# Optimization experiments

Hardware: AMD Instinct MI355X
Metric: run time of the kernel (lower is better)

The kernel has to match this reference:

```python
import jax, jax.numpy as jnp
import numpy as np

SCALE = 64.0 ** -0.5  # dim ** -0.5
H, D = 8, 8  # heads, head_dim (dim = 64)


def setup_inputs() -> dict:
    key = jax.random.key(0)
    ks = jax.random.split(key, 5)
    b, n, dim = 4, 2048, 64
    return {
        "x": jax.random.normal(ks[0], (b, n, dim), dtype=jnp.float32),
        "Wqkv": jax.random.normal(ks[1], (dim, 3 * dim), dtype=jnp.float32) * 0.05,
        "bqkv": jax.random.normal(ks[2], (3 * dim,), dtype=jnp.float32) * 0.05,
        "W1": jax.random.normal(ks[3], (dim, dim), dtype=jnp.float32) * 0.05,
        "b1": jax.random.normal(ks[4], (dim,), dtype=jnp.float32) * 0.05,
    }


def reference(x, Wqkv, bqkv, W1, b1):
    b, n, dim = x.shape
    # --- stage 1: standard multi-head attention ---
    qkv = x @ Wqkv + bqkv  # [b, n, 3*dim]
    q, k, v = jnp.split(qkv, 3, axis=-1)
    # rearrange 'b n (h d) -> b h n d'
    split = lambda t: t.reshape(b, n, H, D).transpose(0, 2, 1, 3)
    q, k, v = split(q), split(k), split(v)
    dots = jnp.einsum('bhid,bhjd->bhij', q, k) * SCALE  # [b,h,n,n]
    attn = jax.nn.softmax(dots, axis=-1)
    out1 = jnp.einsum('bhij,bhjd->bhid', attn, v)
    out = out1.transpose(0, 2, 1, 3).reshape(b, n, dim)  # 'b h n d -> b n (h d)'
    # --- stage 2: second attention on nn1 projection (same weights => q1=k1=v1) ---
    p = out @ W1 + b1  # [b, n, 64]
    # torch: q1.view(b, 8, n, 8) -- a raw reshape, NOT a head split
    q1 = p.reshape(b, 8, n, 8)
    dots1 = jnp.einsum('bhid,bhjd->bhij', q1, q1) * SCALE  # [b,8,n,n]
    attn1 = jax.nn.softmax(dots1, axis=-1)
    out2 = jnp.einsum('bhij,bhjd->bhid', attn1, q1)
    # torch: rearrange 'b h n d -> b n (h d)'
    out2 = out2.transpose(0, 2, 1, 3).reshape(b, n, dim)
    out2 = out2 @ W1 + b1
    # dropout is identity in eval mode
    return out2
```

## Files before the change

kernel.cpp:

```cpp
#include <hip/hip_runtime.h>

typedef __attribute__((ext_vector_type(8))) short s8v;
typedef __attribute__((ext_vector_type(4))) short s4v;
typedef __attribute__((ext_vector_type(4))) float fx4;
typedef unsigned short u16;
typedef unsigned int u32;
typedef unsigned char u8;

#define QK_SCALE 0.1803368801111204f

#if __has_builtin(__builtin_amdgcn_exp2f)
#define EXP2(x) __builtin_amdgcn_exp2f(x)
#else
#define EXP2(x) exp2f(x)
#endif

static __device__ __forceinline__ u16 f2bf(float f) {
    u32 u = __float_as_uint(f);
    u += 0x7fffu + ((u >> 16) & 1u);
    return (u16)(u >> 16);
}
static __device__ __forceinline__ float bf2f(u16 h) {
    return __uint_as_float(((u32)h) << 16);
}
static __device__ __forceinline__ int packtrunc(float a, float b) {
    return (int)__builtin_amdgcn_perm(__float_as_uint(b), __float_as_uint(a), 0x07060302u);
}

static __device__ __forceinline__ fx4 mfma16(s4v a, s4v b, fx4 c) {
#if __has_builtin(__builtin_amdgcn_mfma_f32_16x16x16bf16_1k)
    return __builtin_amdgcn_mfma_f32_16x16x16bf16_1k(a, b, c, 0, 0, 0);
#else
    asm("v_mfma_f32_16x16x16_bf16 %0, %1, %2, %3" : "=v"(c) : "v"(a), "v"(b), "v"(c));
    return c;
#endif
}

__global__ __launch_bounds__(192) void qkv_proj_kernel(
    const float* __restrict__ X, const float* __restrict__ W,
    const float* __restrict__ bias,
    u16* __restrict__ Qh, u16* __restrict__ Kh, u16* __restrict__ Vt,
    u32* __restrict__ VtBoth)
{
    {
        const int gt = blockIdx.x * 192 + threadIdx.x;
        #pragma unroll
        for (int i = 0; i < 3; ++i) {
            const int idx = gt + i * 196608;
            if (idx < 524288) {
                const int region = idx >> 6, word = idx & 63;
                VtBoth[region * 128 + 64 + word] = (word < 8) ? 0x3f803f80u : 0u;
            }
        }
    }
    __shared__ __align__(16) float xsT[64 * 12];
    const int row0 = blockIdx.x * 8;
    const int t = threadIdx.x;
    if (t < 64) {
        #pragma unroll
        for (int r = 0; r < 8; ++r)
            xsT[t * 12 + r] = X[(size_t)(row0 + r) * 64 + t];
    }
    __syncthreads();
    const int j = t;
    const float bj = bias[j];
    float acc[8];
    #pragma unroll
    for (int r = 0; r < 8; ++r) acc[r] = bj;
    #pragma unroll 4
    for (int k = 0; k < 64; ++k) {
        const float w = W[k * 192 + j];
        const float4 x0 = *(const float4*)&xsT[k * 12];
        const float4 x1 = *(const float4*)&xsT[k * 12 + 4];
        acc[0] = fmaf(x0.x, w, acc[0]);
        acc[1] = fmaf(x0.y, w, acc[1]);
        acc[2] = fmaf(x0.z, w, acc[2]);
        acc[3] = fmaf(x0.w, w, acc[3]);
        acc[4] = fmaf(x1.x, w, acc[4]);
        acc[5] = fmaf(x1.y, w, acc[5]);
        acc[6] = fmaf(x1.z, w, acc[6]);
        acc[7] = fmaf(x1.w, w, acc[7]);
    }
    const int c = j & 63;
    const int h = c >> 3, d = c & 7;
    #pragma unroll
    for (int r = 0; r < 8; ++r) {
        const int R = row0 + r;
        const int bi = R >> 11, i = R & 2047;
        const int bh = bi * 8 + h;
        const float v = acc[r];
        if (j < 64) {
            const float qs = v * QK_SCALE;
            const u16 hh = f2bf(qs);
            const u16 ll = f2bf(qs - bf2f(hh));
            u16* qp = Qh + ((size_t)(bh * 2048 + i)) * 16 + d;
            qp[0] = hh; qp[8] = ll;
        } else if (j < 128) {
            const u16 hh = f2bf(v);
            const u16 ll = f2bf(v - bf2f(hh));
            u16* kp = Kh + ((size_t)(bh * 128 + (i >> 4)) * 16 + (i & 15)) * 16 + d;
            kp[0] = hh; kp[8] = ll;
        } else {
            Vt[((size_t)(bh * 128 + (i >> 4)) * 16 + d) * 16 + (i & 15)] = f2bf(v);
        }
    }
}

__global__ __launch_bounds__(256, 4) void attn_mfma5_kernel(
    const u16* __restrict__ Qh, const u8* __restrict__ Khb,
    const u8* __restrict__ Vtb, float* __restrict__ Part)
{
    __shared__ __align__(16) float Lr[4][4][64][4];
    const int bh = blockIdx.x, qt = blockIdx.y, sp = blockIdx.z;
    const int tid = threadIdx.x, w = tid >> 6, l = tid & 63;
    const int g = l >> 4, ql = l & 15;

    s8v bq[4];
    #pragma unroll
    for (int qg = 0; qg < 4; ++qg)
        bq[qg] = *(const s8v*)(Qh + ((size_t)(bh * 2048 + qt * 64 + qg * 16 + ql)) * 16
                               + (g >> 1) * 8);

    const size_t kvoff = (size_t)bh * 65536 + sp * 32768 + w * 8192;
    const u8* kptr = Khb + kvoff + ql * 32 + (g & 1) * 16;
    const u8* vptr = Vtb + kvoff + ql * 32 + g * 8;

    fx4 acc0 = {0.f, 0.f, 0.f, 0.f}, acc1 = acc0, acc2 = acc0, acc3 = acc0;
    const fx4 zf = {0.f, 0.f, 0.f, 0.f};

    s8v k0 = *(const s8v*)(kptr);
    s8v k1 = *(const s8v*)(kptr + 512);
    s4v v0 = *(const s4v*)(vptr);
    s4v v1 = *(const s4v*)(vptr + 512);

#define QK_COMPUTE(KA, VA)                                                      \
    {                                                                           \
        _Pragma("unroll")                                                       \
        for (int qg = 0; qg < 4; ++qg) {                                        \
            fx4 s = __builtin_amdgcn_mfma_f32_16x16x32_bf16(KA, bq[qg], zf, 0, 0, 0); \
            const float e0 = EXP2(s[0]), e1 = EXP2(s[1]);                       \
            const float e2 = EXP2(s[2]), e3 = EXP2(s[3]);                       \
            union { int i[2]; s4v v; } bp;                                      \
            bp.i[0] = packtrunc(e0, e1);                                        \
            bp.i[1] = packtrunc(e2, e3);                                        \
            fx4& acc = (qg == 0) ? acc0 : (qg == 1) ? acc1 : (qg == 2) ? acc2 : acc3; \
            acc = mfma16(VA, bp.v, acc);                                        \
        }                                                                       \
    }

    #pragma unroll 1
    for (int seg = 0; seg < 16; seg += 2) {
        const s8v k2 = *(const s8v*)(kptr + (seg + 2) * 512);
        const s4v v2 = *(const s4v*)(vptr + (seg + 2) * 512);
        const s8v k3 = *(const s8v*)(kptr + (seg + 3) * 512);
        const s4v v3 = *(const s4v*)(vptr + (seg + 3) * 512);
        QK_COMPUTE(k0, v0);
        QK_COMPUTE(k1, v1);
        k0 = k2; v0 = v2; k1 = k3; v1 = v3;
    }
#undef QK_COMPUTE

    *(fx4*)&Lr[w][0][l][0] = acc0;
    *(fx4*)&Lr[w][1][l][0] = acc1;
    *(fx4*)&Lr[w][2][l][0] = acc2;
    *(fx4*)&Lr[w][3][l][0] = acc3;
    __syncthreads();
    fx4 fin = {0.f, 0.f, 0.f, 0.f};
    #pragma unroll
    for (int wp = 0; wp < 4; ++wp) {
        const fx4 v = *(const fx4*)&Lr[wp][w][l][0];
        fin[0] += v[0]; fin[1] += v[1]; fin[2] += v[2]; fin[3] += v[3];
    }

    const int qglob = qt * 64 + w * 16 + ql;
    float* pp = Part + ((size_t)(bh * 2048 + qglob)) * 24 + sp * 12;
    if (g < 2) {
        const float4 o = {fin[0], fin[1], fin[2], fin[3]};
        *(float4*)(pp + g * 4) = o;
    } else if (g == 2) {
        pp[8] = fin[0];
    }
}

__global__ __launch_bounds__(256) void attn_combine2_kernel(
    const float* __restrict__ Part, float* __restrict__ M)
{
    const int idx = blockIdx.x * 256 + threadIdx.x;
    const float* pp = Part + (size_t)idx * 24;
    const float inv = 1.0f / (pp[8] + pp[20]);
    float o[8];
    #pragma unroll
    for (int d = 0; d < 8; ++d) o[d] = (pp[d] + pp[12 + d]) * inv;
    const int bh = idx >> 11, q = idx & 2047;
    const int b = bh >> 3, h = bh & 7;
    float* op = M + ((size_t)(b * 2048 + q)) * 64 + h * 8;
    const float4 o0 = {o[0], o[1], o[2], o[3]};
    const float4 o1 = {o[4], o[5], o[6], o[7]};
    *(float4*)op = o0;
    *(float4*)(op + 4) = o1;
}

__global__ __launch_bounds__(64) void proj64_kernel(
    const float* __restrict__ X, const float* __restrict__ W,
    const float* __restrict__ bias,
    u16* __restrict__ Qh, u16* __restrict__ Kh, u16* __restrict__ Vt,
    float* __restrict__ Out, int mode)
{
    __shared__ __align__(16) float xsT[64 * 12];
    const int row0 = blockIdx.x * 8;
    const int c = threadIdx.x;
    #pragma unroll
    for (int r = 0; r < 8; ++r)
        xsT[c * 12 + r] = X[(size_t)(row0 + r) * 64 + c];
    __syncthreads();
    const float bc = bias[c];
    float acc[8];
    #pragma unroll
    for (int r = 0; r < 8; ++r) acc[r] = bc;
    #pragma unroll 4
    for (int k = 0; k < 64; ++k) {
        const float w = W[k * 64 + c];
        const float4 x0 = *(const float4*)&xsT[k * 12];
        const float4 x1 = *(const float4*)&xsT[k * 12 + 4];
        acc[0] = fmaf(x0.x, w, acc[0]);
        acc[1] = fmaf(x0.y, w, acc[1]);
        acc[2] = fmaf(x0.z, w, acc[2]);
        acc[3] = fmaf(x0.w, w, acc[3]);
        acc[4] = fmaf(x1.x, w, acc[4]);
        acc[5] = fmaf(x1.y, w, acc[5]);
        acc[6] = fmaf(x1.z, w, acc[6]);
        acc[7] = fmaf(x1.w, w, acc[7]);
    }
    if (mode == 0) {
        #pragma unroll
        for (int r = 0; r < 8; ++r) {
            const int R = row0 + r;
            const int bi = R >> 11, rr = R & 2047;
            const int bh = bi * 8 + (rr >> 8);
            const int key = (rr & 255) * 8 + (c >> 3);
            const int d = c & 7;
            const int kg = key >> 4, kr = key & 15;
            const float p = acc[r];
            const float qs = p * QK_SCALE;
            const u16 qh = f2bf(qs);
            const u16 qlo = f2bf(qs - bf2f(qh));
            const u16 kh = f2bf(p);
            const u16 kl = f2bf(p - bf2f(kh));
            u16* qp = Qh + ((size_t)(bh * 2048 + key)) * 16 + d;
            qp[0] = qh; qp[8] = qlo;
            u16* kp = Kh + ((size_t)(bh * 128 + kg) * 16 + kr) * 16 + d;
            kp[0] = kh; kp[8] = kl;
            Vt[((size_t)(bh * 128 + kg) * 16 + d) * 16 + kr] = f2bf(p);
        }
    } else {
        #pragma unroll
        for (int r = 0; r < 8; ++r)
            Out[(size_t)(row0 + r) * 64 + c] = acc[r];
    }
}

extern "C" void kernel_launch(void* const* d_in, const int* in_sizes, int n_in,
                              void* d_out, int out_size, void* d_ws, size_t ws_size,
                              hipStream_t stream) {
    const float* x    = (const float*)d_in[0];
    const float* Wqkv = (const float*)d_in[1];
    const float* bqkv = (const float*)d_in[2];
    const float* W1   = (const float*)d_in[3];
    const float* b1   = (const float*)d_in[4];
    float* out = (float*)d_out;
    u8* w8 = (u8*)d_ws;

    u16*   Qh0  = (u16*)(w8);
    u16*   Kh0  = (u16*)(w8 + (2u << 20));
    u16*   Vt0  = (u16*)(w8 + (4u << 20));
    u16*   Vt1  = (u16*)(w8 + (6u << 20));
    u16*   Qh1  = (u16*)(w8 + (8u << 20));
    u16*   Kh1  = (u16*)(w8 + (10u << 20));
    float* Part = (float*)(w8 + (12u << 20));
    float* M1   = (float*)(w8 + (18u << 20));
    float* M2   = (float*)(w8);

    qkv_proj_kernel<<<1024, 192, 0, stream>>>(x, Wqkv, bqkv, Qh0, Kh0, Vt0, (u32*)Vt0);
    attn_mfma5_kernel<<<dim3(32, 32, 2), 256, 0, stream>>>(Qh0, (const u8*)Kh0, (const u8*)Vt0, Part);
    attn_combine2_kernel<<<256, 256, 0, stream>>>(Part, M1);
    proj64_kernel<<<1024, 64, 0, stream>>>(M1, W1, b1, Qh1, Kh1, Vt1, nullptr, 0);
    attn_mfma5_kernel<<<dim3(32, 32, 2), 256, 0, stream>>>(Qh1, (const u8*)Kh1, (const u8*)Vt1, Part);
    attn_combine2_kernel<<<256, 256, 0, stream>>>(Part, M2);
    proj64_kernel<<<1024, 64, 0, stream>>>(M2, W1, b1, nullptr, nullptr, nullptr, out, 1);
}
```

Measured before the change: 72.95 us.

## Drop KV split-K and fuse softmax normalization into attention kernel

```diff
diff --git a/kernel.cpp b/kernel.cpp
--- a/kernel.cpp
+++ b/kernel.cpp
@@ -30,6 +30,8 @@
 static __device__ __forceinline__ fx4 mfma16(s4v a, s4v b, fx4 c) {
 #if __has_builtin(__builtin_amdgcn_mfma_f32_16x16x16bf16_1k)
     return __builtin_amdgcn_mfma_f32_16x16x16bf16_1k(a, b, c, 0, 0, 0);
+#elif __has_builtin(__builtin_amdgcn_mfma_f32_16x16x16_bf16)
+    return __builtin_amdgcn_mfma_f32_16x16x16_bf16(a, b, c, 0, 0, 0);
 #else
     asm("v_mfma_f32_16x16x16_bf16 %0, %1, %2, %3" : "=v"(c) : "v"(a), "v"(b), "v"(c));
     return c;
@@ -106,26 +108,28 @@
     }
 }
 
-__global__ __launch_bounds__(256, 4) void attn_mfma5_kernel(
+__global__ __launch_bounds__(256, 8) void attn_mfma9_kernel(
     const u16* __restrict__ Qh, const u8* __restrict__ Khb,
-    const u8* __restrict__ Vtb, float* __restrict__ Part)
+    const u8* __restrict__ Vtb, float* __restrict__ M)
 {
-    __shared__ __align__(16) float Lr[4][4][64][4];
-    const int bh = blockIdx.x, qt = blockIdx.y, sp = blockIdx.z;
+    __shared__ __align__(16) float Lr[4][2][64][4];
+    const int bh = blockIdx.x, qt = blockIdx.y;
     const int tid = threadIdx.x, w = tid >> 6, l = tid & 63;
     const int g = l >> 4, ql = l & 15;
 
-    s8v bq[4];
-    #pragma unroll
-    for (int qg = 0; qg < 4; ++qg)
-        bq[qg] = *(const s8v*)(Qh + ((size_t)(bh * 2048 + qt * 64 + qg * 16 + ql)) * 16
+    s8v bq[2];
+    #pragma unroll
+    for (int qg = 0; qg < 2; ++qg)
+        bq[qg] = *(const s8v*)(Qh + ((size_t)(bh * 2048 + qt * 32 + qg * 16 + ql)) * 16
                                + (g >> 1) * 8);
 
-    const size_t kvoff = (size_t)bh * 65536 + sp * 32768 + w * 8192;
+    const size_t kvoff = (size_t)bh * 65536 + w * 16384;
     const u8* kptr = Khb + kvoff + ql * 32 + (g & 1) * 16;
     const u8* vptr = Vtb + kvoff + ql * 32 + g * 8;
 
-    fx4 acc0 = {0.f, 0.f, 0.f, 0.f}, acc1 = acc0, acc2 = acc0, acc3 = acc0;
+    fx4 acc[2];
+    acc[0] = fx4{0.f, 0.f, 0.f, 0.f};
+    acc[1] = fx4{0.f, 0.f, 0.f, 0.f};
     const fx4 zf = {0.f, 0.f, 0.f, 0.f};
 
     s8v k0 = *(const s8v*)(kptr);
@@ -133,71 +137,50 @@
     s4v v0 = *(const s4v*)(vptr);
     s4v v1 = *(const s4v*)(vptr + 512);
 
-#define QK_COMPUTE(KA, VA)                                                      \
+#define PROCESS(KA, VA)                                                         \
     {                                                                           \
         _Pragma("unroll")                                                       \
-        for (int qg = 0; qg < 4; ++qg) {                                        \
+        for (int qg = 0; qg < 2; ++qg) {                                        \
             fx4 s = __builtin_amdgcn_mfma_f32_16x16x32_bf16(KA, bq[qg], zf, 0, 0, 0); \
-            const float e0 = EXP2(s[0]), e1 = EXP2(s[1]);                       \
-            const float e2 = EXP2(s[2]), e3 = EXP2(s[3]);                       \
-            union { int i[2]; s4v v; } bp;                                      \
-            bp.i[0] = packtrunc(e0, e1);                                        \
-            bp.i[1] = packtrunc(e2, e3);                                        \
-            fx4& acc = (qg == 0) ? acc0 : (qg == 1) ? acc1 : (qg == 2) ? acc2 : acc3; \
-            acc = mfma16(VA, bp.v, acc);                                        \
+            union { int i2[2]; s4v v; } bp;                                     \
+            bp.i2[0] = packtrunc(EXP2(s[0]), EXP2(s[1]));                       \
+            bp.i2[1] = packtrunc(EXP2(s[2]), EXP2(s[3]));                       \
+            acc[qg] = mfma16(VA, bp.v, acc[qg]);                                \
         }                                                                       \
     }
 
     #pragma unroll 1
-    for (int seg = 0; seg < 16; seg += 2) {
+    for (int seg = 0; seg < 32; seg += 2) {
         const s8v k2 = *(const s8v*)(kptr + (seg + 2) * 512);
         const s4v v2 = *(const s4v*)(vptr + (seg + 2) * 512);
         const s8v k3 = *(const s8v*)(kptr + (seg + 3) * 512);
         const s4v v3 = *(const s4v*)(vptr + (seg + 3) * 512);
-        QK_COMPUTE(k0, v0);
-        QK_COMPUTE(k1, v1);
+        PROCESS(k0, v0);
+        PROCESS(k1, v1);
         k0 = k2; v0 = v2; k1 = k3; v1 = v3;
     }
-#undef QK_COMPUTE
-
-    *(fx4*)&Lr[w][0][l][0] = acc0;
-    *(fx4*)&Lr[w][1][l][0] = acc1;
-    *(fx4*)&Lr[w][2][l][0] = acc2;
-    *(fx4*)&Lr[w][3][l][0] = acc3;
+#undef PROCESS
+
+    *(fx4*)&Lr[w][0][l][0] = acc[0];
+    *(fx4*)&Lr[w][1][l][0] = acc[1];
     __syncthreads();
-    fx4 fin = {0.f, 0.f, 0.f, 0.f};
-    #pragma unroll
-    for (int wp = 0; wp < 4; ++wp) {
-        const fx4 v = *(const fx4*)&Lr[wp][w][l][0];
-        fin[0] += v[0]; fin[1] += v[1]; fin[2] += v[2]; fin[3] += v[3];
-    }
-
-    const int qglob = qt * 64 + w * 16 + ql;
-    float* pp = Part + ((size_t)(bh * 2048 + qglob)) * 24 + sp * 12;
-    if (g < 2) {
-        const float4 o = {fin[0], fin[1], fin[2], fin[3]};
-        *(float4*)(pp + g * 4) = o;
-    } else if (g == 2) {
-        pp[8] = fin[0];
-    }
-}
-
-__global__ __launch_bounds__(256) void attn_combine2_kernel(
-    const float* __restrict__ Part, float* __restrict__ M)
-{
-    const int idx = blockIdx.x * 256 + threadIdx.x;
-    const float* pp = Part + (size_t)idx * 24;
-    const float inv = 1.0f / (pp[8] + pp[20]);
-    float o[8];
-    #pragma unroll
-    for (int d = 0; d < 8; ++d) o[d] = (pp[d] + pp[12 + d]) * inv;
-    const int bh = idx >> 11, q = idx & 2047;
-    const int b = bh >> 3, h = bh & 7;
-    float* op = M + ((size_t)(b * 2048 + q)) * 64 + h * 8;
-    const float4 o0 = {o[0], o[1], o[2], o[3]};
-    const float4 o1 = {o[4], o[5], o[6], o[7]};
-    *(float4*)op = o0;
-    *(float4*)(op + 4) = o1;
+
+    if (w < 2) {
+        fx4 fin = {0.f, 0.f, 0.f, 0.f};
+        #pragma unroll
+        for (int wp = 0; wp < 4; ++wp) {
+            const fx4 v = *(const fx4*)&Lr[wp][w][l][0];
+            fin[0] += v[0]; fin[1] += v[1]; fin[2] += v[2]; fin[3] += v[3];
+        }
+        const int lv_i = __builtin_amdgcn_ds_bpermute((32 + ql) * 4, __float_as_int(fin[0]));
+        const float inv = 1.0f / __int_as_float(lv_i);
+        if (g < 2) {
+            const int qglob = qt * 32 + w * 16 + ql;
+            const int b = bh >> 3, h = bh & 7;
+            const float4 o = {fin[0] * inv, fin[1] * inv, fin[2] * inv, fin[3] * inv};
+            *(float4*)(M + ((size_t)(b * 2048 + qglob)) * 64 + h * 8 + g * 4) = o;
+        }
+    }
 }
 
 __global__ __launch_bounds__(64) void proj64_kernel(
@@ -276,15 +259,12 @@
     u16*   Vt1  = (u16*)(w8 + (6u << 20));
     u16*   Qh1  = (u16*)(w8 + (8u << 20));
     u16*   Kh1  = (u16*)(w8 + (10u << 20));
-    float* Part = (float*)(w8 + (12u << 20));
-    float* M1   = (float*)(w8 + (18u << 20));
+    float* M1   = (float*)(w8 + (12u << 20));
     float* M2   = (float*)(w8);
 
     qkv_proj_kernel<<<1024, 192, 0, stream>>>(x, Wqkv, bqkv, Qh0, Kh0, Vt0, (u32*)Vt0);
-    attn_mfma5_kernel<<<dim3(32, 32, 2), 256, 0, stream>>>(Qh0, (const u8*)Kh0, (const u8*)Vt0, Part);
-    attn_combine2_kernel<<<256, 256, 0, stream>>>(Part, M1);
+    attn_mfma9_kernel<<<dim3(32, 64), 256, 0, stream>>>(Qh0, (const u8*)Kh0, (const u8*)Vt0, M1);
     proj64_kernel<<<1024, 64, 0, stream>>>(M1, W1, b1, Qh1, Kh1, Vt1, nullptr, 0);
-    attn_mfma5_kernel<<<dim3(32, 32, 2), 256, 0, stream>>>(Qh1, (const u8*)Kh1, (const u8*)Vt1, Part);
-    attn_combine2_kernel<<<256, 256, 0, stream>>>(Part, M2);
+    attn_mfma9_kernel<<<dim3(32, 64), 256, 0, stream>>>(Qh1, (const u8*)Kh1, (const u8*)Vt1, M2);
     proj64_kernel<<<1024, 64, 0, stream>>>(M2, W1, b1, nullptr, nullptr, nullptr, out, 1);
 }
```

Result: faster. 64.20 us (-12.0%).
